# Kernel tuning notes

Hardware: AMD Instinct MI355X
Metric: run time of the kernel (lower is better)

Reference implementation:

```python
import jax, jax.numpy as jnp
import numpy as np

EPS = 1e-8
NEG = -1e7  # min_val used by masked_max


def _div_safe(a, b):
    return a / jnp.maximum(b, EPS)


def _masked_max(v, m, axis):
    mb = jnp.broadcast_to(m, v.shape)
    val = jnp.where(mb > 0, v, NEG).max(axis=axis)
    return val * mb.max(axis=axis)


def _masked_mean(v, m, axis):
    mb = jnp.broadcast_to(m, v.shape)
    return _div_safe((v * mb).sum(axis=axis), mb.sum(axis=axis))


def _cos_pairwise(v1, v2):
    # v1: (b,p,h), v2: (b,q,h) -> (b,p,q)
    n1 = jnp.linalg.norm(v1, axis=2, keepdims=True)
    n2 = jnp.linalg.norm(v2, axis=2, keepdims=True)
    dot = jnp.einsum('bph,bqh->bpq', v1, v2)
    return _div_safe(dot, n1 * n2.transpose(0, 2, 1))


def _mpm(v1, v2, w):
    # v1,v2: (b,L,h); w: (np,h) -> ((b,L,1), (b,L,np))
    dot = (v1 * v2).sum(-1)
    n = jnp.linalg.norm(v1, axis=-1) * jnp.linalg.norm(v2, axis=-1)
    mv1 = _div_safe(dot, n)[..., None]
    wv1 = w[None, None] * v1[:, :, None, :]  # (b,L,np,h)
    wv2 = w[None, None] * v2[:, :, None, :]
    dotm = (wv1 * wv2).sum(-1)
    nm = jnp.linalg.norm(wv1, axis=-1) * jnp.linalg.norm(wv2, axis=-1)
    return mv1, _div_safe(dotm, nm)


def _mpm_pairwise(v1, v2, w):
    # v1: (b,L1,h), v2: (b,L2,h), w: (np,h) -> (b,L1,L2,np)
    wv1 = w[None, :, None, :] * v1[:, None, :, :]  # (b,np,L1,h)
    wv2 = w[None, :, None, :] * v2[:, None, :, :]  # (b,np,L2,h)
    n1 = jnp.linalg.norm(wv1, axis=3, keepdims=True)
    n2 = jnp.linalg.norm(wv2, axis=3, keepdims=True)
    dot = jnp.einsum('bnph,bnqh->bnpq', wv1, wv2)
    res = _div_safe(dot, n1 * n2.transpose(0, 1, 3, 2))
    return res.transpose(0, 2, 3, 1)


def _bimpm(context_p, mask_p, context_h, mask_h, w_full, w_maxpool, w_att, w_max_att):
    b = context_p.shape[0]
    mask_p_h = mask_p[:, :, None] * mask_h[:, None, :]  # (b,Lp,Lh)
    mask_h_p = mask_p_h.transpose(0, 2, 1)
    context_p = context_p * mask_p[:, :, None]
    context_h = context_h * mask_h[:, :, None]

    cos = _cos_pairwise(context_p, context_h)  # (b,Lp,Lh)
    mv_p = [_masked_max(cos, mask_p_h, 2)[:, :, None],
            _masked_mean(cos, mask_p_h, 2)[:, :, None]]
    cos_t = cos.transpose(0, 2, 1)
    mv_h = [_masked_max(cos_t, mask_h_p, 2)[:, :, None],
            _masked_mean(cos_t, mask_h_p, 2)[:, :, None]]

    # full match (is_forward=True): match against last non-pad token
    idx_p = jnp.clip(mask_p.sum(1).astype(jnp.int32) - 1, 0)
    idx_h = jnp.clip(mask_h.sum(1).astype(jnp.int32) - 1, 0)
    last_p = context_p[jnp.arange(b), idx_p][:, None, :]  # (b,1,h)
    last_h = context_h[jnp.arange(b), idx_h][:, None, :]
    m1, mm = _mpm(context_p, jnp.broadcast_to(last_h, context_p.shape), w_full)
    mv_p += [m1, mm]
    m1, mm = _mpm(context_h, jnp.broadcast_to(last_p, context_h.shape), w_full)
    mv_h += [m1, mm]

    # maxpool match
    mv_max = _mpm_pairwise(context_p, context_h, w_maxpool)  # (b,Lp,Lh,np)
    mv_p += [_masked_max(mv_max, mask_p_h[..., None], 2),
             _masked_mean(mv_max, mask_p_h[..., None], 2)]
    mv_max_t = mv_max.transpose(0, 2, 1, 3)
    mv_h += [_masked_max(mv_max_t, mask_h_p[..., None], 2),
             _masked_mean(mv_max_t, mask_h_p[..., None], 2)]

    # attentive match
    att_h = context_h[:, None, :, :] * cos[..., None]  # (b,Lp,Lh,h)
    att_p = context_p[:, :, None, :] * cos[..., None]  # (b,Lp,Lh,h)
    att_mean_h = _div_safe(jnp.einsum('bpq,bqh->bph', cos, context_h),
                           cos.sum(2, keepdims=True))
    att_mean_p = _div_safe(jnp.einsum('bpq,bph->bqh', cos, context_p),
                           cos.sum(1, keepdims=True).transpose(0, 2, 1))
    m1, mm = _mpm(context_p, att_mean_h, w_att)
    mv_p += [m1, mm]
    m1, mm = _mpm(context_h, att_mean_p, w_att)
    mv_h += [m1, mm]

    # max attentive match
    att_max_h = _masked_max(att_h, mask_p_h[..., None], 2)  # (b,Lp,h)
    att_max_p = _masked_max(att_p.transpose(0, 2, 1, 3), mask_h_p[..., None], 2)  # (b,Lh,h)
    m1, mm = _mpm(context_p, att_max_h, w_max_att)
    mv_p += [m1, mm]
    m1, mm = _mpm(context_h, att_max_p, w_max_att)
    mv_h += [m1, mm]

    return jnp.concatenate(mv_p, axis=2), jnp.concatenate(mv_h, axis=2)


def setup_inputs() -> dict:
    B, LP, LH, H, NP = 32, 128, 128, 200, 20
    key = jax.random.key(0)
    ks = jax.random.split(key, 8)
    len_p = jax.random.randint(ks[0], (B,), LP // 2, LP + 1)
    len_h = jax.random.randint(ks[1], (B,), LH // 2, LH + 1)
    return {
        'context_p': jax.random.normal(ks[2], (B, LP, H), dtype=jnp.float32),
        'mask_p': (jnp.arange(LP)[None, :] < len_p[:, None]).astype(jnp.float32),
        'context_h': jax.random.normal(ks[3], (B, LH, H), dtype=jnp.float32),
        'mask_h': (jnp.arange(LH)[None, :] < len_h[:, None]).astype(jnp.float32),
        'w_full': jax.random.uniform(ks[4], (NP, H), dtype=jnp.float32),
        'w_maxpool': jax.random.uniform(ks[5], (NP, H), dtype=jnp.float32),
        'w_att': jax.random.uniform(ks[6], (NP, H), dtype=jnp.float32),
        'w_max_att': jax.random.uniform(ks[7], (NP, H), dtype=jnp.float32),
    }


def reference(context_p, mask_p, context_h, mask_h, w_full, w_maxpool, w_att, w_max_att):
    return _bimpm(context_p, mask_p, context_h, mask_h, w_full, w_maxpool, w_att, w_max_att)
```

## Files before the change

### kernel.cpp

```cpp
#include <hip/hip_runtime.h>
#include <hip/hip_bf16.h>


#define EPSF 1e-8f
#define NEGF -1e7f

constexpr int Bc = 32, Lc = 128, Hc = 200, NPc = 20, NCHc = 105;
constexpr int KP = 224;
constexpr size_t SLL = (size_t)Bc * Lc * Lc;

constexpr size_t OFF_COS    = 0;
constexpr size_t OFF_COST   = OFF_COS + SLL;
constexpr size_t OFF_NORMP  = OFF_COST + SLL;
constexpr size_t OFF_NORMH  = OFF_NORMP + (size_t)Bc * Lc;
constexpr size_t OFF_LENP   = OFF_NORMH + (size_t)Bc * Lc;
constexpr size_t OFF_LENH   = OFF_LENP + Bc;
constexpr size_t OFF_LASTP  = OFF_LENH + Bc;
constexpr size_t OFF_LASTH  = OFF_LASTP + (size_t)Bc * Hc;
constexpr size_t OFF_NWP    = OFF_LASTH + (size_t)Bc * Hc;
constexpr size_t OFF_NWH    = OFF_NWP + (size_t)Bc * NPc * Lc;
constexpr size_t OFF_MASKPF = OFF_NWH + (size_t)Bc * NPc * Lc;
constexpr size_t OFF_MASKHF = OFF_MASKPF + (size_t)Bc * Lc;
constexpr size_t OFF_FLAG   = OFF_MASKHF + (size_t)Bc * Lc;
constexpr size_t OFF_WT     = OFF_FLAG + 64;
constexpr size_t OFF_RPMAX  = OFF_WT + (size_t)Hc * 64;
constexpr size_t OFF_RPSUM  = OFF_RPMAX + 2 * (size_t)Bc * NPc * Lc;
constexpr size_t OFF_CPMAX  = OFF_RPSUM + 2 * (size_t)Bc * NPc * Lc;
constexpr size_t OFF_CPSUM  = OFF_CPMAX + 2 * (size_t)Bc * NPc * Lc;
constexpr size_t OFF_CHB    = OFF_CPSUM + 2 * (size_t)Bc * NPc * Lc;
constexpr size_t OFF_CPB    = OFF_CHB + ((size_t)Bc * Lc * KP) / 2;
constexpr size_t OFF_W2K    = OFF_CPB + ((size_t)Bc * Lc * KP) / 2;
constexpr size_t WS_FLOATS  = OFF_W2K + (size_t)NPc * KP;

typedef __attribute__((ext_vector_type(8))) short short8v;
typedef __attribute__((ext_vector_type(4))) float float4v;
typedef __attribute__((ext_vector_type(2))) float float2v;

__device__ __forceinline__ float loadf(const void* p, size_t i, int isb) {
  if (isb) return __bfloat162float(((const __hip_bfloat16*)p)[i]);
  return ((const float*)p)[i];
}

__device__ __forceinline__ void storef(void* out, size_t i, float v, int isb) {
  if (isb) ((__hip_bfloat16*)out)[i] = __float2bfloat16(v);
  else ((float*)out)[i] = v;
}

__device__ __forceinline__ float s2f(unsigned short s) {
  union { unsigned u; float f; } c;
  c.u = ((unsigned)s) << 16;
  return c.f;
}

__device__ __forceinline__ short b2s(float f) {
  __hip_bfloat16 h = __float2bfloat16(f);
  union { __hip_bfloat16 b; short s; } u;
  u.b = h;
  return u.s;
}

__device__ __forceinline__ short8v weight8(short8v a, float4v w0, float4v w1) {
  short8v r;
#pragma unroll
  for (int e = 0; e < 8; e++) {
    float w = (e < 4) ? w0[e] : w1[e - 4];
    r[e] = b2s(s2f((unsigned short)a[e]) * w);
  }
  return r;
}

__global__ __launch_bounds__(256) void prep_kernel(
    const void* __restrict__ cp_, const void* __restrict__ mp,
    const void* __restrict__ ch_, const void* __restrict__ mh,
    const void* __restrict__ wf, const void* __restrict__ wmp,
    const void* __restrict__ watt, const void* __restrict__ wma,
    float* __restrict__ ws) {
  int isb = (((const unsigned short*)mp)[0] == 0x3F80u) ? 1 : 0;
  int bid = blockIdx.x;
  int t = threadIdx.x;
  const int n0 = Bc * Lc;
  if (bid < 2048) {
    int g = bid * 4 + (t >> 6);
    int side = g >> 12;
    int bl = g & 4095;
    int b = bl >> 7, l = bl & 127;
    int lane = t & 63;
    const void* ctx = side ? ch_ : cp_;
    const void* maskin = side ? mh : mp;
    float mk = loadf(maskin, b * Lc + l, isb);
    size_t rowbase = ((size_t)b * Lc + l) * Hc;
    __hip_bfloat16* cb16 = (__hip_bfloat16*)(ws + (side ? OFF_CHB : OFF_CPB));
    size_t cb = ((size_t)b * Lc + l) * KP;

    float v[4];
    float ss = 0.f;
    for (int i = 0; i < 4; i++) {
      int h = lane + 64 * i;
      float x = 0.f;
      if (h < Hc) {
        x = loadf(ctx, rowbase + h, isb) * mk;
        cb16[cb + h] = __float2bfloat16(x);
      } else if (h < KP) {
        cb16[cb + h] = __float2bfloat16(0.f);
      }
      v[i] = x;
      ss += x * x;
    }
    for (int o = 32; o > 0; o >>= 1) ss += __shfl_xor(ss, o);
    if (lane == 0) ws[(side ? OFF_NORMH : OFF_NORMP) + b * Lc + l] = sqrtf(ss);

    float* nw = ws + (side ? OFF_NWH : OFF_NWP) + (size_t)b * NPc * Lc;
    for (int np_ = 0; np_ < NPc; np_++) {
      float s = 0.f;
      for (int i = 0; i < 4; i++) {
        int h = lane + 64 * i;
        if (h < Hc) {
          float w = loadf(wmp, (size_t)np_ * Hc + h, isb);
          float wx = w * v[i];
          s += wx * wx;
        }
      }
      for (int o = 32; o > 0; o >>= 1) s += __shfl_xor(s, o);
      if (lane == 0) nw[np_ * Lc + l] = sqrtf(s);
    }
    return;
  }
  int cb = bid - 2048;
  if (cb >= 100) {
    int idx = (cb - 100) * 4 + (t >> 6);
    int side = idx >> 5, b = idx & 31;
    int lane = t & 63;
    const void* mask = side ? mh : mp;
    const void* ctx = side ? ch_ : cp_;
    float s = 0.f;
    for (int l = lane; l < Lc; l += 64) s += loadf(mask, b * Lc + l, isb);
    for (int o = 32; o > 0; o >>= 1) s += __shfl_xor(s, o);
    if (lane == 0) ws[(side ? OFF_LENH : OFF_LENP) + b] = s;
    int lidx = (int)(s + 0.5f) - 1;
    if (lidx < 0) lidx = 0;
    float mk = loadf(mask, b * Lc + lidx, isb);
    float* lastv = ws + (side ? OFF_LASTH : OFF_LASTP) + (size_t)b * Hc;
    for (int h = lane; h < Hc; h += 64)
      lastv[h] = loadf(ctx, ((size_t)b * Lc + lidx) * Hc + h, isb) * mk;
    return;
  }
  int g = cb * 256 + t;
  if (g == 0) ws[OFF_FLAG] = (float)isb;
  if (g < n0) {
    ws[OFF_MASKPF + g] = loadf(mp, g, isb);
  } else if (g < 2 * n0) {
    ws[OFF_MASKHF + (g - n0)] = loadf(mh, g - n0, isb);
  } else if (g < 2 * n0 + 64 * Hc) {
    int r = g - 2 * n0;
    int h = r >> 6, c = r & 63;
    float w = 1.0f;
    if (c < 20) w = loadf(wf, (size_t)c * Hc + h, isb);
    else if (c < 40) w = loadf(watt, (size_t)(c - 20) * Hc + h, isb);
    else if (c < 60) w = loadf(wma, (size_t)(c - 40) * Hc + h, isb);
    ws[OFF_WT + r] = w * w;
  } else if (g < 2 * n0 + 64 * Hc + NPc * KP) {
    int r = g - (2 * n0 + 64 * Hc);
    int np_ = r / KP, k = r % KP;
    float w = (k < Hc) ? loadf(wmp, (size_t)np_ * Hc + k, isb) : 0.f;
    ws[OFF_W2K + r] = w * w;
  }
}

__global__ __launch_bounds__(64, 3) void maxpool_kernel(float* __restrict__ ws) {
  int b = blockIdx.x;
  int s = blockIdx.y;
  int np_ = blockIdx.z;
  int pi = s >> 1, qi = s & 1;
  int cosmode = (np_ == NPc);
  int lane = threadIdx.x;
  int rsel = lane & 15, quad = lane >> 4;

  const short* Ab = (const short*)(ws + OFF_CPB)
                  + ((size_t)b * Lc + pi * 64 + rsel) * KP + quad * 8;
  const short* Bb = (const short*)(ws + OFF_CHB)
                  + ((size_t)b * Lc + qi * 64 + rsel) * KP + quad * 8;
  const float* w2k = ws + OFF_W2K + (size_t)(cosmode ? 0 : np_) * KP + quad * 8;

  float4v acc[4][4];
  float4v zf = {0.f, 0.f, 0.f, 0.f};
#pragma unroll
  for (int i = 0; i < 4; i++)
#pragma unroll
    for (int j = 0; j < 4; j++) acc[i][j] = zf;

#pragma unroll
  for (int st = 0; st < 7; st++) {
    int k0 = st * 32;
    short8v bf4[4], af[4];
#pragma unroll
    for (int t = 0; t < 4; t++)
      bf4[t] = *(const short8v*)(Bb + (size_t)t * 16 * KP + k0);
    if (cosmode) {
#pragma unroll
      for (int t = 0; t < 4; t++)
        af[t] = *(const short8v*)(Ab + (size_t)t * 16 * KP + k0);
    } else {
      float4v w0 = *(const float4v*)(w2k + k0);
      float4v w1 = *(const float4v*)(w2k + k0 + 4);
#pragma unroll
      for (int t = 0; t < 4; t++) {
        short8v ar = *(const short8v*)(Ab + (size_t)t * 16 * KP + k0);
        af[t] = weight8(ar, w0, w1);
      }
    }
#pragma unroll
    for (int i = 0; i < 4; i++)
#pragma unroll
      for (int j = 0; j < 4; j++)
        acc[i][j] = __builtin_amdgcn_mfma_f32_16x16x32_bf16(af[i], bf4[j], acc[i][j], 0, 0, 0);
  }

  if (cosmode) {
    const float* npn = ws + OFF_NORMP + b * Lc + pi * 64;
    const float* nhn = ws + OFF_NORMH + b * Lc + qi * 64;
    float nh4[4];
#pragma unroll
    for (int tj = 0; tj < 4; tj++) nh4[tj] = nhn[tj * 16 + rsel];
    float* cosp = ws + OFF_COS + (size_t)b * Lc * Lc;
    float* cost = ws + OFF_COST + (size_t)b * Lc * Lc;
#pragma unroll
    for (int ti = 0; ti < 4; ti++) {
#pragma unroll
      for (int r = 0; r < 4; r++) {
        int prow = pi * 64 + ti * 16 + quad * 4 + r;
        float npv = npn[ti * 16 + quad * 4 + r];
#pragma unroll
        for (int tj = 0; tj < 4; tj++) {
          int qcol = qi * 64 + tj * 16 + rsel;
          float v = acc[ti][tj][r] * __builtin_amdgcn_rcpf(fmaxf(npv * nh4[tj], EPSF));
          cosp[(size_t)prow * Lc + qcol] = v;
          cost[(size_t)qcol * Lc + prow] = v;
        }
      }
    }
    return;
  }

  const float* nwp = ws + OFF_NWP + ((size_t)b * NPc + np_) * Lc + pi * 64;
  const float* nwh = ws + OFF_NWH + ((size_t)b * NPc + np_) * Lc + qi * 64;
  const float* maskP = ws + OFF_MASKPF + b * Lc + pi * 64;
  const float* maskH = ws + OFF_MASKHF + b * Lc + qi * 64;
  float nhv[4], mhv[4], cmax[4], csum[4];
#pragma unroll
  for (int tj = 0; tj < 4; tj++) {
    int q = tj * 16 + rsel;
    nhv[tj] = nwh[q];
    mhv[tj] = maskH[q];
    cmax[tj] = NEGF;
    csum[tj] = 0.f;
  }
  size_t rbase = (((size_t)qi * Bc + b) * NPc + np_) * Lc + pi * 64;
  size_t cbase = (((size_t)pi * Bc + b) * NPc + np_) * Lc + qi * 64;
#pragma unroll
  for (int ti = 0; ti < 4; ti++) {
#pragma unroll
    for (int r = 0; r < 4; r++) {
      int p = ti * 16 + quad * 4 + r;
      float npv = nwp[p], mpv = maskP[p];
      float rm = NEGF, rs = 0.f;
#pragma unroll
      for (int tj = 0; tj < 4; tj++) {
        float v = acc[ti][tj][r] * __builtin_amdgcn_rcpf(fmaxf(npv * nhv[tj], EPSF));
        if (mhv[tj] > 0.f) rm = fmaxf(rm, v);
        rs += v * mhv[tj];
        if (mpv > 0.f) cmax[tj] = fmaxf(cmax[tj], v);
        csum[tj] += v * mpv;
      }
#pragma unroll
      for (int o = 1; o <= 8; o <<= 1) {
        rm = fmaxf(rm, __shfl_xor(rm, o));
        rs += __shfl_xor(rs, o);
      }
      if (rsel == 0) {
        ws[OFF_RPMAX + rbase + p] = rm;
        ws[OFF_RPSUM + rbase + p] = rs;
      }
    }
  }
#pragma unroll
  for (int tj = 0; tj < 4; tj++) {
#pragma unroll
    for (int o = 16; o <= 32; o <<= 1) {
      cmax[tj] = fmaxf(cmax[tj], __shfl_xor(cmax[tj], o));
      csum[tj] += __shfl_xor(csum[tj], o);
    }
  }
  if (quad == 0) {
#pragma unroll
    for (int tj = 0; tj < 4; tj++) {
      int q = tj * 16 + rsel;
      ws[OFF_CPMAX + cbase + q] = cmax[tj];
      ws[OFF_CPSUM + cbase + q] = csum[tj];
    }
  }
}

__global__ __launch_bounds__(256) void attmpm_kernel(float* __restrict__ ws,
                                                     void* __restrict__ out) {
  int b = blockIdx.x;
  int r0 = blockIdx.y * 4;
  int side = blockIdx.z;
  int t = threadIdx.x;
  int isb = ws[OFF_FLAG] > 0.5f;
  const float* cosrows = ws + (side ? OFF_COST : OFF_COS) + ((size_t)b * Lc + r0) * Lc;
  const unsigned short* vsb = (const unsigned short*)(ws + (side ? OFF_CPB : OFF_CHB))
                            + (size_t)b * Lc * KP;
  const unsigned short* v1b = (const unsigned short*)(ws + (side ? OFF_CHB : OFF_CPB))
                            + ((size_t)b * Lc + r0) * KP;
  const float* vlast = ws + (side ? OFF_LASTP : OFF_LASTH) + (size_t)b * Hc;
  const float* maskRow = ws + (side ? OFF_MASKHF : OFF_MASKPF) + b * Lc;
  float lenOther = ws[(side ? OFF_LENP : OFF_LENH) + b];
  int lenO = (int)(lenOther + 0.5f);
  size_t obase = (size_t)side * Bc * Lc * NCHc + ((size_t)b * Lc + r0) * NCHc;

  __shared__ float crowT[Lc][4];
  __shared__ float dens[4];
  __shared__ float v1s[4][Hc];
  __shared__ float v2l[Hc];
  __shared__ float am[4][Hc];
  __shared__ float ax[4][Hc];
  for (int i = t; i < 4 * Lc; i += 256) {
    int row = i >> 7, q = i & 127;
    crowT[q][row] = cosrows[(size_t)row * Lc + q];
  }
  for (int i = t; i < 4 * Hc; i += 256) {
    int row = i / Hc, h = i % Hc;
    v1s[row][h] = s2f(v1b[(size_t)row * KP + h]);
  }
  for (int h = t; h < Hc; h += 256) v2l[h] = vlast[h];
  __syncthreads();

  int wv = t >> 6, lane = t & 63;
  {
    float x1 = crowT[lane][wv], x2 = crowT[lane + 64][wv];
    float sv = x1 + x2;
    float mv = fmaxf(x1, (lane + 64 < lenO) ? x2 : NEGF);
    for (int o = 32; o > 0; o >>= 1) {
      sv += __shfl_xor(sv, o);
      mv = fmaxf(mv, __shfl_xor(mv, o));
    }
    if (lane == 0) {
      dens[wv] = sv;
      float mr = maskRow[r0 + wv];
      storef(out, obase + (size_t)wv * NCHc + 0, mr * mv, isb);
      storef(out, obase + (size_t)wv * NCHc + 1, mr * sv / fmaxf(mr * lenOther, EPSF), isb);
    }
  }
  __syncthreads();

  if (t < Hc) {
    float2v s01 = {0.f, 0.f}, s23 = {0.f, 0.f};
    float2v m01 = {NEGF, NEGF}, m23 = {NEGF, NEGF};
    const unsigned short* vb = vsb + t;
    int q = 0;
    for (; q + 8 <= lenO; q += 8) {
      unsigned short raw[8];
#pragma unroll
      for (int j = 0; j < 8; j++) raw[j] = vb[(size_t)(q + j) * KP];
      float4 cc[8];
#pragma unroll
      for (int j = 0; j < 8; j++) cc[j] = *(const float4*)&crowT[q + j][0];
#pragma unroll
      for (int j = 0; j < 8; j++) {
        float pr = s2f(raw[j]);
        float2v pp = {pr, pr};
        float2v c01 = {cc[j].x, cc[j].y}, c23 = {cc[j].z, cc[j].w};
        float2v v01 = c01 * pp, v23 = c23 * pp;
        s01 += v01;
        s23 += v23;
        m01[0] = fmaxf(m01[0], v01[0]); m01[1] = fmaxf(m01[1], v01[1]);
        m23[0] = fmaxf(m23[0], v23[0]); m23[1] = fmaxf(m23[1], v23[1]);
      }
    }
    for (; q < lenO; q++) {
      float pr = s2f(vb[(size_t)q * KP]);
      float4 c4 = *(const float4*)&crowT[q][0];
      float2v pp = {pr, pr};
      float2v c01 = {c4.x, c4.y}, c23 = {c4.z, c4.w};
      float2v v01 = c01 * pp, v23 = c23 * pp;
      s01 += v01;
      s23 += v23;
      m01[0] = fmaxf(m01[0], v01[0]); m01[1] = fmaxf(m01[1], v01[1]);
      m23[0] = fmaxf(m23[0], v23[0]); m23[1] = fmaxf(m23[1], v23[1]);
    }
    am[0][t] = s01[0] / fmaxf(dens[0], EPSF);
    am[1][t] = s01[1] / fmaxf(dens[1], EPSF);
    am[2][t] = s23[0] / fmaxf(dens[2], EPSF);
    am[3][t] = s23[1] / fmaxf(dens[3], EPSF);
    ax[0][t] = maskRow[r0 + 0] * m01[0];
    ax[1][t] = maskRow[r0 + 1] * m01[1];
    ax[2][t] = maskRow[r0 + 2] * m23[0];
    ax[3][t] = maskRow[r0 + 3] * m23[1];
  }
  __syncthreads();

  int c = lane;
  int row = r0 + wv;
  size_t orow = obase + (size_t)wv * NCHc;

  if (c < NPc) {
    size_t PMX = side ? OFF_CPMAX : OFF_RPMAX;
    size_t PSM = side ? OFF_CPSUM : OFF_RPSUM;
    size_t i0 = (((size_t)0 * Bc + b) * NPc + c) * Lc + row;
    size_t i1 = (((size_t)1 * Bc + b) * NPc + c) * Lc + row;
    float m = fmaxf(ws[PMX + i0], ws[PMX + i1]);
    float sum = ws[PSM + i0] + ws[PSM + i1];
    float mk = maskRow[row];
    storef(out, orow + 23 + c, mk * m, isb);
    storef(out, orow + 43 + c, mk * sum / fmaxf(mk * lenOther, EPSF), isb);
  }

  int v2i = (c < 20) ? 0 : (c < 40) ? 1 : (c < 60) ? 2 : (c - 60);
  if (v2i > 2) v2i = 2;
  const float* y = (v2i == 0) ? v2l : (v2i == 1) ? am[wv] : ax[wv];
  const float* x = v1s[wv];
  const float* wtc = ws + OFF_WT + c;
  float2v sd = {0.f, 0.f}, sa = {0.f, 0.f}, sb = {0.f, 0.f};
#pragma unroll 2
  for (int h4 = 0; h4 < Hc / 4; h4++) {
    float w0 = wtc[(size_t)(h4 * 4 + 0) * 64];
    float w1 = wtc[(size_t)(h4 * 4 + 1) * 64];
    float w2 = wtc[(size_t)(h4 * 4 + 2) * 64];
    float w3 = wtc[(size_t)(h4 * 4 + 3) * 64];
    float4 xv = *(const float4*)&x[h4 * 4];
    float4 yv = *(const float4*)&y[h4 * 4];
    float2v wq0 = {w0, w1}, wq1 = {w2, w3};
    float2v x0 = {xv.x, xv.y}, x1 = {xv.z, xv.w};
    float2v y0 = {yv.x, yv.y}, y1 = {yv.z, yv.w};
    float2v t0 = wq0 * x0;
    sd += t0 * y0; sa += t0 * x0; sb += wq0 * (y0 * y0);
    t0 = wq1 * x1;
    sd += t0 * y1; sa += t0 * x1; sb += wq1 * (y1 * y1);
  }
  float sdf = sd[0] + sd[1], saf = sa[0] + sa[1], sbf = sb[0] + sb[1];
  float mm = sdf / fmaxf(sqrtf(saf) * sqrtf(sbf), EPSF);
  int ch;
  if (c < 20) ch = 3 + c;
  else if (c < 40) ch = 64 + (c - 20);
  else if (c < 60) ch = 85 + (c - 40);
  else if (c == 60) ch = 2;
  else if (c == 61) ch = 63;
  else if (c == 62) ch = 84;
  else ch = -1;
  if (ch >= 0) storef(out, orow + ch, mm, isb);
}

extern "C" void kernel_launch(void* const* d_in, const int* in_sizes, int n_in,
                              void* d_out, int out_size, void* d_ws, size_t ws_size,
                              hipStream_t stream) {
  const void* ctx_p = d_in[0];
  const void* mask_p = d_in[1];
  const void* ctx_h = d_in[2];
  const void* mask_h = d_in[3];
  const void* w_full = d_in[4];
  const void* w_mp = d_in[5];
  const void* w_att = d_in[6];
  const void* w_maxatt = d_in[7];
  float* ws = (float*)d_ws;

  prep_kernel<<<2164, 256, 0, stream>>>(ctx_p, mask_p, ctx_h, mask_h,
                                        w_full, w_mp, w_att, w_maxatt, ws);
  maxpool_kernel<<<dim3(Bc, 4, NPc + 1), 64, 0, stream>>>(ws);
  attmpm_kernel<<<dim3(Bc, Lc / 4, 2), 256, 0, stream>>>(ws, d_out);
}
```

Before: 153.1 us.

## Split attentive reduction across all threads and transpose weight table layout

```diff
diff --git a/kernel.cpp b/kernel.cpp
--- a/kernel.cpp
+++ b/kernel.cpp
@@ -110,18 +110,29 @@
     if (lane == 0) ws[(side ? OFF_NORMH : OFF_NORMP) + b * Lc + l] = sqrtf(ss);
 
     float* nw = ws + (side ? OFF_NWH : OFF_NWP) + (size_t)b * NPc * Lc;
+    float s[NPc];
+#pragma unroll
     for (int np_ = 0; np_ < NPc; np_++) {
-      float s = 0.f;
+      float acc = 0.f;
+#pragma unroll
       for (int i = 0; i < 4; i++) {
         int h = lane + 64 * i;
         if (h < Hc) {
           float w = loadf(wmp, (size_t)np_ * Hc + h, isb);
           float wx = w * v[i];
-          s += wx * wx;
+          acc += wx * wx;
         }
       }
-      for (int o = 32; o > 0; o >>= 1) s += __shfl_xor(s, o);
-      if (lane == 0) nw[np_ * Lc + l] = sqrtf(s);
+      s[np_] = acc;
+    }
+#pragma unroll
+    for (int o = 32; o > 0; o >>= 1) {
+#pragma unroll
+      for (int np_ = 0; np_ < NPc; np_++) s[np_] += __shfl_xor(s[np_], o);
+    }
+    if (lane == 0) {
+#pragma unroll
+      for (int np_ = 0; np_ < NPc; np_++) nw[np_ * Lc + l] = sqrtf(s[np_]);
     }
     return;
   }
@@ -152,7 +163,7 @@
     ws[OFF_MASKHF + (g - n0)] = loadf(mh, g - n0, isb);
   } else if (g < 2 * n0 + 64 * Hc) {
     int r = g - 2 * n0;
-    int h = r >> 6, c = r & 63;
+    int c = r / Hc, h = r - c * Hc;
     float w = 1.0f;
     if (c < 20) w = loadf(wf, (size_t)c * Hc + h, isb);
     else if (c < 40) w = loadf(watt, (size_t)(c - 20) * Hc + h, isb);
@@ -322,8 +333,8 @@
   __shared__ float dens[4];
   __shared__ float v1s[4][Hc];
   __shared__ float v2l[Hc];
-  __shared__ float am[4][Hc];
-  __shared__ float ax[4][Hc];
+  __shared__ float am2[2][4][Hc];
+  __shared__ float ax2[2][4][Hc];
   for (int i = t; i < 4 * Lc; i += 256) {
     int row = i >> 7, q = i & 127;
     crowT[q][row] = cosrows[(size_t)row * Lc + q];
@@ -353,49 +364,80 @@
   }
   __syncthreads();
 
+  {
+    int half = t >> 7;
+    int tt = t & 127;
+    int len2 = (lenO + 1) >> 1;
+    int qbeg = half ? len2 : 0;
+    int qend = half ? lenO : len2;
+    if (tt < 100) {
+      int c0 = tt * 2;
+      const unsigned short* vb = vsb + c0;
+      float2v s0 = {0.f, 0.f}, s1 = {0.f, 0.f}, s2 = {0.f, 0.f}, s3 = {0.f, 0.f};
+      float2v m0 = {NEGF, NEGF}, m1 = {NEGF, NEGF}, m2 = {NEGF, NEGF}, m3 = {NEGF, NEGF};
+      int q = qbeg;
+      for (; q + 8 <= qend; q += 8) {
+        unsigned raw[8];
+#pragma unroll
+        for (int j = 0; j < 8; j++)
+          raw[j] = *(const unsigned*)(vb + (size_t)(q + j) * KP);
+        float4 cc[8];
+#pragma unroll
+        for (int j = 0; j < 8; j++) cc[j] = *(const float4*)&crowT[q + j][0];
+#pragma unroll
+        for (int j = 0; j < 8; j++) {
+          union { unsigned u; float f; } lo, hi;
+          lo.u = raw[j] << 16;
+          hi.u = raw[j] & 0xFFFF0000u;
+          float2v pv = {lo.f, hi.f};
+          float2v v;
+          v = pv * (float2v){cc[j].x, cc[j].x};
+          s0 += v; m0[0] = fmaxf(m0[0], v[0]); m0[1] = fmaxf(m0[1], v[1]);
+          v = pv * (float2v){cc[j].y, cc[j].y};
+          s1 += v; m1[0] = fmaxf(m1[0], v[0]); m1[1] = fmaxf(m1[1], v[1]);
+          v = pv * (float2v){cc[j].z, cc[j].z};
+          s2 += v; m2[0] = fmaxf(m2[0], v[0]); m2[1] = fmaxf(m2[1], v[1]);
+          v = pv * (float2v){cc[j].w, cc[j].w};
+          s3 += v; m3[0] = fmaxf(m3[0], v[0]); m3[1] = fmaxf(m3[1], v[1]);
+        }
+      }
+      for (; q < qend; q++) {
+        unsigned r2 = *(const unsigned*)(vb + (size_t)q * KP);
+        union { unsigned u; float f; } lo, hi;
+        lo.u = r2 << 16;
+        hi.u = r2 & 0xFFFF0000u;
+        float2v pv = {lo.f, hi.f};
+        float4 c4 = *(const float4*)&crowT[q][0];
+        float2v v;
+        v = pv * (float2v){c4.x, c4.x};
+        s0 += v; m0[0] = fmaxf(m0[0], v[0]); m0[1] = fmaxf(m0[1], v[1]);
+        v = pv * (float2v){c4.y, c4.y};
+        s1 += v; m1[0] = fmaxf(m1[0], v[0]); m1[1] = fmaxf(m1[1], v[1]);
+        v = pv * (float2v){c4.z, c4.z};
+        s2 += v; m2[0] = fmaxf(m2[0], v[0]); m2[1] = fmaxf(m2[1], v[1]);
+        v = pv * (float2v){c4.w, c4.w};
+        s3 += v; m3[0] = fmaxf(m3[0], v[0]); m3[1] = fmaxf(m3[1], v[1]);
+      }
+      *(float2v*)&am2[half][0][c0] = s0;
+      *(float2v*)&am2[half][1][c0] = s1;
+      *(float2v*)&am2[half][2][c0] = s2;
+      *(float2v*)&am2[half][3][c0] = s3;
+      *(float2v*)&ax2[half][0][c0] = m0;
+      *(float2v*)&ax2[half][1][c0] = m1;
+      *(float2v*)&ax2[half][2][c0] = m2;
+      *(float2v*)&ax2[half][3][c0] = m3;
+    }
+  }
+  __syncthreads();
+
   if (t < Hc) {
-    float2v s01 = {0.f, 0.f}, s23 = {0.f, 0.f};
-    float2v m01 = {NEGF, NEGF}, m23 = {NEGF, NEGF};
-    const unsigned short* vb = vsb + t;
-    int q = 0;
-    for (; q + 8 <= lenO; q += 8) {
-      unsigned short raw[8];
-#pragma unroll
-      for (int j = 0; j < 8; j++) raw[j] = vb[(size_t)(q + j) * KP];
-      float4 cc[8];
-#pragma unroll
-      for (int j = 0; j < 8; j++) cc[j] = *(const float4*)&crowT[q + j][0];
-#pragma unroll
-      for (int j = 0; j < 8; j++) {
-        float pr = s2f(raw[j]);
-        float2v pp = {pr, pr};
-        float2v c01 = {cc[j].x, cc[j].y}, c23 = {cc[j].z, cc[j].w};
-        float2v v01 = c01 * pp, v23 = c23 * pp;
-        s01 += v01;
-        s23 += v23;
-        m01[0] = fmaxf(m01[0], v01[0]); m01[1] = fmaxf(m01[1], v01[1]);
-        m23[0] = fmaxf(m23[0], v23[0]); m23[1] = fmaxf(m23[1], v23[1]);
-      }
-    }
-    for (; q < lenO; q++) {
-      float pr = s2f(vb[(size_t)q * KP]);
-      float4 c4 = *(const float4*)&crowT[q][0];
-      float2v pp = {pr, pr};
-      float2v c01 = {c4.x, c4.y}, c23 = {c4.z, c4.w};
-      float2v v01 = c01 * pp, v23 = c23 * pp;
-      s01 += v01;
-      s23 += v23;
-      m01[0] = fmaxf(m01[0], v01[0]); m01[1] = fmaxf(m01[1], v01[1]);
-      m23[0] = fmaxf(m23[0], v23[0]); m23[1] = fmaxf(m23[1], v23[1]);
-    }
-    am[0][t] = s01[0] / fmaxf(dens[0], EPSF);
-    am[1][t] = s01[1] / fmaxf(dens[1], EPSF);
-    am[2][t] = s23[0] / fmaxf(dens[2], EPSF);
-    am[3][t] = s23[1] / fmaxf(dens[3], EPSF);
-    ax[0][t] = maskRow[r0 + 0] * m01[0];
-    ax[1][t] = maskRow[r0 + 1] * m01[1];
-    ax[2][t] = maskRow[r0 + 2] * m23[0];
-    ax[3][t] = maskRow[r0 + 3] * m23[1];
+#pragma unroll
+    for (int r = 0; r < 4; r++) {
+      float sv = am2[0][r][t] + am2[1][r][t];
+      am2[0][r][t] = sv / fmaxf(dens[r], EPSF);
+      float xv = fmaxf(ax2[0][r][t], ax2[1][r][t]);
+      ax2[0][r][t] = maskRow[r0 + r] * xv;
+    }
   }
   __syncthreads();
 
@@ -417,19 +459,16 @@
 
   int v2i = (c < 20) ? 0 : (c < 40) ? 1 : (c < 60) ? 2 : (c - 60);
   if (v2i > 2) v2i = 2;
-  const float* y = (v2i == 0) ? v2l : (v2i == 1) ? am[wv] : ax[wv];
+  const float* y = (v2i == 0) ? v2l : (v2i == 1) ? am2[0][wv] : ax2[0][wv];
   const float* x = v1s[wv];
-  const float* wtc = ws + OFF_WT + c;
+  const float* wtc = ws + OFF_WT + (size_t)c * Hc;
   float2v sd = {0.f, 0.f}, sa = {0.f, 0.f}, sb = {0.f, 0.f};
 #pragma unroll 2
   for (int h4 = 0; h4 < Hc / 4; h4++) {
-    float w0 = wtc[(size_t)(h4 * 4 + 0) * 64];
-    float w1 = wtc[(size_t)(h4 * 4 + 1) * 64];
-    float w2 = wtc[(size_t)(h4 * 4 + 2) * 64];
-    float w3 = wtc[(size_t)(h4 * 4 + 3) * 64];
+    float4 wq = *(const float4*)&wtc[h4 * 4];
     float4 xv = *(const float4*)&x[h4 * 4];
     float4 yv = *(const float4*)&y[h4 * 4];
-    float2v wq0 = {w0, w1}, wq1 = {w2, w3};
+    float2v wq0 = {wq.x, wq.y}, wq1 = {wq.z, wq.w};
     float2v x0 = {xv.x, xv.y}, x1 = {xv.z, xv.w};
     float2v y0 = {yv.x, yv.y}, y1 = {yv.z, yv.w};
     float2v t0 = wq0 * x0;
```

Result: slower. 159.8 us (+4.4%).

## Pack four perspectives per maxpool block and batch prep norm reductions

Applied to the files above, without the earlier changes.

```diff
diff --git a/kernel.cpp b/kernel.cpp
--- a/kernel.cpp
+++ b/kernel.cpp
@@ -110,18 +110,29 @@
     if (lane == 0) ws[(side ? OFF_NORMH : OFF_NORMP) + b * Lc + l] = sqrtf(ss);
 
     float* nw = ws + (side ? OFF_NWH : OFF_NWP) + (size_t)b * NPc * Lc;
+    float s[NPc];
+#pragma unroll
     for (int np_ = 0; np_ < NPc; np_++) {
-      float s = 0.f;
+      float acc = 0.f;
+#pragma unroll
       for (int i = 0; i < 4; i++) {
         int h = lane + 64 * i;
         if (h < Hc) {
           float w = loadf(wmp, (size_t)np_ * Hc + h, isb);
           float wx = w * v[i];
-          s += wx * wx;
+          acc += wx * wx;
         }
       }
-      for (int o = 32; o > 0; o >>= 1) s += __shfl_xor(s, o);
-      if (lane == 0) nw[np_ * Lc + l] = sqrtf(s);
+      s[np_] = acc;
+    }
+#pragma unroll
+    for (int o = 32; o > 0; o >>= 1) {
+#pragma unroll
+      for (int np_ = 0; np_ < NPc; np_++) s[np_] += __shfl_xor(s[np_], o);
+    }
+    if (lane == 0) {
+#pragma unroll
+      for (int np_ = 0; np_ < NPc; np_++) nw[np_ * Lc + l] = sqrtf(s[np_]);
     }
     return;
   }
@@ -166,20 +177,23 @@
   }
 }
 
-__global__ __launch_bounds__(64, 3) void maxpool_kernel(float* __restrict__ ws) {
+__global__ __launch_bounds__(256) void maxpool4_kernel(float* __restrict__ ws) {
   int b = blockIdx.x;
   int s = blockIdx.y;
-  int np_ = blockIdx.z;
+  int z = blockIdx.z;
+  int wv = threadIdx.x >> 6;
+  int lane = threadIdx.x & 63;
+  int cosmode = (z == 5);
+  if (cosmode && wv != 0) return;
+  int np_ = cosmode ? 0 : z * 4 + wv;
   int pi = s >> 1, qi = s & 1;
-  int cosmode = (np_ == NPc);
-  int lane = threadIdx.x;
   int rsel = lane & 15, quad = lane >> 4;
 
   const short* Ab = (const short*)(ws + OFF_CPB)
                   + ((size_t)b * Lc + pi * 64 + rsel) * KP + quad * 8;
   const short* Bb = (const short*)(ws + OFF_CHB)
                   + ((size_t)b * Lc + qi * 64 + rsel) * KP + quad * 8;
-  const float* w2k = ws + OFF_W2K + (size_t)(cosmode ? 0 : np_) * KP + quad * 8;
+  const float* w2k = ws + OFF_W2K + (size_t)np_ * KP + quad * 8;
 
   float4v acc[4][4];
   float4v zf = {0.f, 0.f, 0.f, 0.f};
@@ -465,6 +479,6 @@
 
   prep_kernel<<<2164, 256, 0, stream>>>(ctx_p, mask_p, ctx_h, mask_h,
                                         w_full, w_mp, w_att, w_maxatt, ws);
-  maxpool_kernel<<<dim3(Bc, 4, NPc + 1), 64, 0, stream>>>(ws);
+  maxpool4_kernel<<<dim3(Bc, 4, 6), 256, 0, stream>>>(ws);
   attmpm_kernel<<<dim3(Bc, Lc / 4, 2), 256, 0, stream>>>(ws, d_out);
 }
```

Measured after the change: 179.8 us. 1.17x slower.

## Precompute w²-weighted bf16 context per perspective in prep kernel

Applied to the files above, without the earlier changes.

```diff
diff --git a/kernel.cpp b/kernel.cpp
--- a/kernel.cpp
+++ b/kernel.cpp
@@ -29,8 +29,8 @@
 constexpr size_t OFF_CPSUM  = OFF_CPMAX + 2 * (size_t)Bc * NPc * Lc;
 constexpr size_t OFF_CHB    = OFF_CPSUM + 2 * (size_t)Bc * NPc * Lc;
 constexpr size_t OFF_CPB    = OFF_CHB + ((size_t)Bc * Lc * KP) / 2;
-constexpr size_t OFF_W2K    = OFF_CPB + ((size_t)Bc * Lc * KP) / 2;
-constexpr size_t WS_FLOATS  = OFF_W2K + (size_t)NPc * KP;
+constexpr size_t OFF_W2A    = OFF_CPB + ((size_t)Bc * Lc * KP) / 2;
+constexpr size_t WS_FLOATS  = OFF_W2A + ((size_t)Bc * NPc * Lc * KP) / 2;
 
 typedef __attribute__((ext_vector_type(8))) short short8v;
 typedef __attribute__((ext_vector_type(4))) float float4v;
@@ -57,16 +57,6 @@
   union { __hip_bfloat16 b; short s; } u;
   u.b = h;
   return u.s;
-}
-
-__device__ __forceinline__ short8v weight8(short8v a, float4v w0, float4v w1) {
-  short8v r;
-#pragma unroll
-  for (int e = 0; e < 8; e++) {
-    float w = (e < 4) ? w0[e] : w1[e - 4];
-    r[e] = b2s(s2f((unsigned short)a[e]) * w);
-  }
-  return r;
 }
 
 __global__ __launch_bounds__(256) void prep_kernel(
@@ -93,35 +83,58 @@
     size_t cb = ((size_t)b * Lc + l) * KP;
 
     float v[4];
+    short xr[4];
     float ss = 0.f;
     for (int i = 0; i < 4; i++) {
       int h = lane + 64 * i;
       float x = 0.f;
+      short xb = 0;
       if (h < Hc) {
         x = loadf(ctx, rowbase + h, isb) * mk;
+        xb = b2s(x);
         cb16[cb + h] = __float2bfloat16(x);
       } else if (h < KP) {
         cb16[cb + h] = __float2bfloat16(0.f);
       }
       v[i] = x;
+      xr[i] = xb;
       ss += x * x;
     }
     for (int o = 32; o > 0; o >>= 1) ss += __shfl_xor(ss, o);
     if (lane == 0) ws[(side ? OFF_NORMH : OFF_NORMP) + b * Lc + l] = sqrtf(ss);
 
     float* nw = ws + (side ? OFF_NWH : OFF_NWP) + (size_t)b * NPc * Lc;
+    __hip_bfloat16* w2a = (__hip_bfloat16*)(ws + OFF_W2A);
+    size_t w2abase = ((size_t)b * NPc) * Lc * KP + (size_t)l * KP;
+    float s[NPc];
+#pragma unroll
     for (int np_ = 0; np_ < NPc; np_++) {
-      float s = 0.f;
+      float acc = 0.f;
+#pragma unroll
       for (int i = 0; i < 4; i++) {
         int h = lane + 64 * i;
         if (h < Hc) {
           float w = loadf(wmp, (size_t)np_ * Hc + h, isb);
           float wx = w * v[i];
-          s += wx * wx;
+          acc += wx * wx;
+          if (side == 0) {
+            w2a[w2abase + (size_t)np_ * Lc * KP + h] =
+                __float2bfloat16(s2f((unsigned short)xr[i]) * (w * w));
+          }
+        } else if (h < KP && side == 0) {
+          w2a[w2abase + (size_t)np_ * Lc * KP + h] = __float2bfloat16(0.f);
         }
       }
-      for (int o = 32; o > 0; o >>= 1) s += __shfl_xor(s, o);
-      if (lane == 0) nw[np_ * Lc + l] = sqrtf(s);
+      s[np_] = acc;
+    }
+#pragma unroll
+    for (int o = 32; o > 0; o >>= 1) {
+#pragma unroll
+      for (int np_ = 0; np_ < NPc; np_++) s[np_] += __shfl_xor(s[np_], o);
+    }
+    if (lane == 0) {
+#pragma unroll
+      for (int np_ = 0; np_ < NPc; np_++) nw[np_ * Lc + l] = sqrtf(s[np_]);
     }
     return;
   }
@@ -158,11 +171,6 @@
     else if (c < 40) w = loadf(watt, (size_t)(c - 20) * Hc + h, isb);
     else if (c < 60) w = loadf(wma, (size_t)(c - 40) * Hc + h, isb);
     ws[OFF_WT + r] = w * w;
-  } else if (g < 2 * n0 + 64 * Hc + NPc * KP) {
-    int r = g - (2 * n0 + 64 * Hc);
-    int np_ = r / KP, k = r % KP;
-    float w = (k < Hc) ? loadf(wmp, (size_t)np_ * Hc + k, isb) : 0.f;
-    ws[OFF_W2K + r] = w * w;
   }
 }
 
@@ -175,11 +183,12 @@
   int lane = threadIdx.x;
   int rsel = lane & 15, quad = lane >> 4;
 
-  const short* Ab = (const short*)(ws + OFF_CPB)
-                  + ((size_t)b * Lc + pi * 64 + rsel) * KP + quad * 8;
+  const short* Ab = cosmode
+      ? (const short*)(ws + OFF_CPB) + ((size_t)b * Lc + pi * 64 + rsel) * KP + quad * 8
+      : (const short*)(ws + OFF_W2A)
+        + (((size_t)b * NPc + np_) * Lc + pi * 64 + rsel) * KP + quad * 8;
   const short* Bb = (const short*)(ws + OFF_CHB)
                   + ((size_t)b * Lc + qi * 64 + rsel) * KP + quad * 8;
-  const float* w2k = ws + OFF_W2K + (size_t)(cosmode ? 0 : np_) * KP + quad * 8;
 
   float4v acc[4][4];
   float4v zf = {0.f, 0.f, 0.f, 0.f};
@@ -193,20 +202,9 @@
     int k0 = st * 32;
     short8v bf4[4], af[4];
 #pragma unroll
-    for (int t = 0; t < 4; t++)
+    for (int t = 0; t < 4; t++) {
       bf4[t] = *(const short8v*)(Bb + (size_t)t * 16 * KP + k0);
-    if (cosmode) {
-#pragma unroll
-      for (int t = 0; t < 4; t++)
-        af[t] = *(const short8v*)(Ab + (size_t)t * 16 * KP + k0);
-    } else {
-      float4v w0 = *(const float4v*)(w2k + k0);
-      float4v w1 = *(const float4v*)(w2k + k0 + 4);
-#pragma unroll
-      for (int t = 0; t < 4; t++) {
-        short8v ar = *(const short8v*)(Ab + (size_t)t * 16 * KP + k0);
-        af[t] = weight8(ar, w0, w1);
-      }
+      af[t] = *(const short8v*)(Ab + (size_t)t * 16 * KP + k0);
     }
 #pragma unroll
     for (int i = 0; i < 4; i++)
```

New measurement: 160.9 us. 5.1% more time.
